# Kernel optimization log

Hardware: AMD Instinct MI355X
Metric: run time of the kernel (lower is better)

## Reference

```python
import jax, jax.numpy as jnp
import numpy as np

B, T, E, H, HD, FF = 2, 2048, 1024, 16, 64, 4096
LN_EPS = 1e-5


def _ln(x, g, b):
    mu = jnp.mean(x, axis=-1, keepdims=True)
    var = jnp.var(x, axis=-1, keepdims=True)
    return (x - mu) * jax.lax.rsqrt(var + LN_EPS) * g + b


def setup_inputs() -> dict:
    key = jax.random.key(0)
    ks = jax.random.split(key, 8)
    s = 0.02
    return {
        "x": jax.random.normal(ks[0], (B, T, E), jnp.float32),
        "Wq": jax.random.normal(ks[1], (H, E, HD), jnp.float32) * s,
        "Wk": jax.random.normal(ks[2], (H, E, HD), jnp.float32) * s,
        "Wv": jax.random.normal(ks[3], (H, E, HD), jnp.float32) * s,
        "Wproj": jax.random.normal(ks[4], (E, E), jnp.float32) * s,
        "bproj": jnp.zeros((E,), jnp.float32),
        "W1": jax.random.normal(ks[5], (E, FF), jnp.float32) * s,
        "b1": jnp.zeros((FF,), jnp.float32),
        "W2": jax.random.normal(ks[6], (FF, E), jnp.float32) * s,
        "b2": jnp.zeros((E,), jnp.float32),
        "g1": jnp.ones((E,), jnp.float32),
        "be1": jnp.zeros((E,), jnp.float32),
        "g2": jnp.ones((E,), jnp.float32),
        "be2": jnp.zeros((E,), jnp.float32),
    }


def reference(x, Wq, Wk, Wv, Wproj, bproj, W1, b1, W2, b2, g1, be1, g2, be2):
    # --- pre-LN multi-head causal self-attention (dropout = eval/identity) ---
    h = _ln(x, g1, be1)  # [B,T,E]
    q = jnp.einsum('btd,hde->bhte', h, Wq)  # [B,H,T,HD]
    k = jnp.einsum('btd,hde->bhte', h, Wk)
    v = jnp.einsum('btd,hde->bhte', h, Wv)
    # NOTE: original code scales by C**-0.5 where C = embedding_dim (not head_size)
    scale = E ** (-0.5)
    wei = jnp.einsum('bhqe,bhke->bhqk', q, k) * scale  # [B,H,T,T]
    causal = jnp.tril(jnp.ones((T, T), dtype=bool))
    wei = jnp.where(causal, wei, -jnp.inf)
    attn = jax.nn.softmax(wei, axis=-1)
    o = jnp.einsum('bhqk,bhke->bhqe', attn, v)  # [B,H,T,HD]
    o = o.transpose(0, 2, 1, 3).reshape(B, T, E)  # concat heads
    o = o @ Wproj + bproj
    x = x + o
    # --- ReLU FFN ---
    h2 = _ln(x, g2, be2)
    f = jax.nn.relu(h2 @ W1 + b1) @ W2 + b2
    return x + f
```

## Files before the change

kernel.cpp:

```cpp
#include <hip/hip_runtime.h>
#include <hip/hip_bf16.h>
#include <stdint.h>

#define T_SEQ 2048
#define E_DIM 1024
#define H_NUM 16
#define HD_DIM 64
#define FF_DIM 4096
#define B_NUM 2
#define N_TOK (B_NUM * T_SEQ)

typedef unsigned short ushort_t;
typedef __bf16 bf16x8 __attribute__((ext_vector_type(8)));
typedef float f32x4 __attribute__((ext_vector_type(4)));

__device__ __forceinline__ float bf2f(ushort_t u) {
    return __uint_as_float(((unsigned)u) << 16);
}
__device__ __forceinline__ ushort_t f2bf(float f) {
    unsigned u = __float_as_uint(f);
    u += 0x7fffu + ((u >> 16) & 1u);
    return (ushort_t)(u >> 16);
}
__device__ __forceinline__ float bflo(unsigned u) { return __uint_as_float(u << 16); }
__device__ __forceinline__ float bfhi(unsigned u) { return __uint_as_float(u & 0xffff0000u); }

__device__ __forceinline__ void async_copy16(const ushort_t* g, ushort_t* l) {
    __builtin_amdgcn_global_load_lds(
        (__attribute__((address_space(1))) uint32_t*)(ushort_t*)g,
        (__attribute__((address_space(3))) uint32_t*)l, 16, 0, 0);
}

__global__ __launch_bounds__(256) void ln_kernel(const float* __restrict__ x,
                                                 const float* __restrict__ g,
                                                 const float* __restrict__ be,
                                                 ushort_t* __restrict__ out) {
    __shared__ float red[8];
    const int row = blockIdx.x, tid = threadIdx.x;
    const float* xr = x + (size_t)row * E_DIM;
    float4 v = ((const float4*)xr)[tid];
    float s = v.x + v.y + v.z + v.w;
    float sq = v.x * v.x + v.y * v.y + v.z * v.z + v.w * v.w;
    for (int off = 32; off; off >>= 1) {
        s += __shfl_xor(s, off);
        sq += __shfl_xor(sq, off);
    }
    const int wid = tid >> 6, lane = tid & 63;
    if (lane == 0) { red[wid] = s; red[4 + wid] = sq; }
    __syncthreads();
    s = red[0] + red[1] + red[2] + red[3];
    sq = red[4] + red[5] + red[6] + red[7];
    const float mean = s * (1.0f / E_DIM);
    const float var = sq * (1.0f / E_DIM) - mean * mean;
    const float rstd = rsqrtf(var + 1e-5f);
    float4 gv = ((const float4*)g)[tid];
    float4 bv = ((const float4*)be)[tid];
    unsigned o0 = f2bf((v.x - mean) * rstd * gv.x + bv.x);
    unsigned o1 = f2bf((v.y - mean) * rstd * gv.y + bv.y);
    unsigned o2 = f2bf((v.z - mean) * rstd * gv.z + bv.z);
    unsigned o3 = f2bf((v.w - mean) * rstd * gv.w + bv.w);
    uint2 w;
    w.x = o0 | (o1 << 16);
    w.y = o2 | (o3 << 16);
    ((uint2*)(out + (size_t)row * E_DIM))[tid] = w;
}

__global__ __launch_bounds__(256) void reduce_ln_kernel(const ushort_t* __restrict__ p0,
                                                        const ushort_t* __restrict__ p1,
                                                        const float* __restrict__ x,
                                                        const float* __restrict__ bias,
                                                        const float* __restrict__ g,
                                                        const float* __restrict__ be,
                                                        float* __restrict__ x1,
                                                        ushort_t* __restrict__ h2) {
    __shared__ float red[8];
    const int row = blockIdx.x, tid = threadIdx.x;
    uint2 u0 = ((const uint2*)(p0 + (size_t)row * E_DIM))[tid];
    uint2 u1 = ((const uint2*)(p1 + (size_t)row * E_DIM))[tid];
    float4 xv = ((const float4*)(x + (size_t)row * E_DIM))[tid];
    float4 bv = ((const float4*)bias)[tid];
    float4 v;
    v.x = xv.x + bv.x + bflo(u0.x) + bflo(u1.x);
    v.y = xv.y + bv.y + bfhi(u0.x) + bfhi(u1.x);
    v.z = xv.z + bv.z + bflo(u0.y) + bflo(u1.y);
    v.w = xv.w + bv.w + bfhi(u0.y) + bfhi(u1.y);
    ((float4*)(x1 + (size_t)row * E_DIM))[tid] = v;
    float s = v.x + v.y + v.z + v.w;
    float sq = v.x * v.x + v.y * v.y + v.z * v.z + v.w * v.w;
    for (int off = 32; off; off >>= 1) {
        s += __shfl_xor(s, off);
        sq += __shfl_xor(sq, off);
    }
    const int wid = tid >> 6, lane = tid & 63;
    if (lane == 0) { red[wid] = s; red[4 + wid] = sq; }
    __syncthreads();
    s = red[0] + red[1] + red[2] + red[3];
    sq = red[4] + red[5] + red[6] + red[7];
    const float mean = s * (1.0f / E_DIM);
    const float var = sq * (1.0f / E_DIM) - mean * mean;
    const float rstd = rsqrtf(var + 1e-5f);
    float4 gv = ((const float4*)g)[tid];
    float4 ev = ((const float4*)be)[tid];
    unsigned o0 = f2bf((v.x - mean) * rstd * gv.x + ev.x);
    unsigned o1 = f2bf((v.y - mean) * rstd * gv.y + ev.y);
    unsigned o2 = f2bf((v.z - mean) * rstd * gv.z + ev.z);
    unsigned o3 = f2bf((v.w - mean) * rstd * gv.w + ev.w);
    uint2 w;
    w.x = o0 | (o1 << 16);
    w.y = o2 | (o3 << 16);
    ((uint2*)(h2 + (size_t)row * E_DIM))[tid] = w;
}

__global__ __launch_bounds__(256) void reduce_out_kernel(const ushort_t* __restrict__ p0,
                                                         const ushort_t* __restrict__ p1,
                                                         const float* __restrict__ x1,
                                                         const float* __restrict__ bias,
                                                         float* __restrict__ out) {
    const int row = blockIdx.x, tid = threadIdx.x;
    uint2 u0 = ((const uint2*)(p0 + (size_t)row * E_DIM))[tid];
    uint2 u1 = ((const uint2*)(p1 + (size_t)row * E_DIM))[tid];
    float4 xv = ((const float4*)(x1 + (size_t)row * E_DIM))[tid];
    float4 bv = ((const float4*)bias)[tid];
    float4 v;
    v.x = xv.x + bv.x + bflo(u0.x) + bflo(u1.x);
    v.y = xv.y + bv.y + bfhi(u0.x) + bfhi(u1.x);
    v.z = xv.z + bv.z + bflo(u0.y) + bflo(u1.y);
    v.w = xv.w + bv.w + bfhi(u0.y) + bfhi(u1.y);
    ((float4*)(out + (size_t)row * E_DIM))[tid] = v;
}

__global__ __launch_bounds__(256) void transpose_kernel(const float* __restrict__ in,
                                                        ushort_t* __restrict__ out,
                                                        int R, int C) {
    __shared__ ushort_t tile[32][33];
    const int c0 = blockIdx.x * 32, r0 = blockIdx.y * 32;
    const int tx = threadIdx.x, ty = threadIdx.y;
#pragma unroll
    for (int i = 0; i < 32; i += 8) tile[ty + i][tx] = f2bf(in[(size_t)(r0 + ty + i) * C + (c0 + tx)]);
    __syncthreads();
#pragma unroll
    for (int i = 0; i < 32; i += 8) out[(size_t)(c0 + ty + i) * R + (r0 + tx)] = tile[tx][ty + i];
}

__global__ __launch_bounds__(256) void transpose_qkv_kernel(const float* __restrict__ Wq,
                                                            const float* __restrict__ Wk,
                                                            const float* __restrict__ Wv,
                                                            ushort_t* __restrict__ outT) {
    __shared__ ushort_t tile[32][33];
    const int z = blockIdx.z, m = z >> 4, hh = z & 15;
    const float* in = ((m == 0) ? Wq : ((m == 1) ? Wk : Wv)) + (size_t)hh * E_DIM * HD_DIM;
    ushort_t* out = outT + (size_t)(m * E_DIM + hh * HD_DIM) * E_DIM;
    const int c0 = blockIdx.x * 32, r0 = blockIdx.y * 32;
    const int tx = threadIdx.x, ty = threadIdx.y;
#pragma unroll
    for (int i = 0; i < 32; i += 8) tile[ty + i][tx] = f2bf(in[(size_t)(r0 + ty + i) * HD_DIM + (c0 + tx)]);
    __syncthreads();
#pragma unroll
    for (int i = 0; i < 32; i += 8) out[(size_t)(c0 + ty + i) * E_DIM + (r0 + tx)] = tile[tx][ty + i];
}

template <int MODE, int BK>
__global__ __launch_bounds__(256) void gemm_bt(const ushort_t* __restrict__ A,
                                               const ushort_t* __restrict__ BT,
                                               const float* __restrict__ bias,
                                               const float* __restrict__ resid,
                                               void* __restrict__ C0,
                                               ushort_t* __restrict__ C1,
                                               ushort_t* __restrict__ C2,
                                               int M, int N, int K, int lda) {
    __shared__ __align__(16) ushort_t lds_a[2][128 * BK];
    __shared__ __align__(16) ushort_t lds_b[2][128 * BK];
    const int tid = threadIdx.x;
    const int id = blockIdx.y * gridDim.x + blockIdx.x;
    const int band = id & 7, within = id >> 3;
    const int rpb = gridDim.y >> 3;
    const int by = band * rpb + (within % rpb);
    const int bx = within / rpb;
    const int m0 = by * 128, n0 = bx * 128;
    const int koff = blockIdx.z * K;
    const int wave = tid >> 6, lane = tid & 63;
    const int wm = (wave >> 1) * 64, wn = (wave & 1) * 64;
    const int quad = lane >> 4, l16 = lane & 15;
    f32x4 acc[4][4] = {};

    const int nk = K / BK;
    auto stage = [&](int kt, int buf) {
        const int k0 = koff + kt * BK;
#pragma unroll
        for (int it = 0; it < BK / 16; ++it) {
            const int ci = it * 256 + tid;
            const int kk = ci >> 9;
            const int rem = ci & 511;
            const int r = rem >> 2, kc = rem & 3;
            const int gk = k0 + kk * 32 + kc * 8;
            async_copy16(A + (size_t)(m0 + r) * lda + gk, &lds_a[buf][ci * 8]);
            async_copy16(BT + (size_t)(n0 + r) * lda + gk, &lds_b[buf][ci * 8]);
        }
    };
    stage(0, 0);

#pragma unroll 1
    for (int kt = 0; kt < nk; ++kt) {
        __syncthreads();
        if (kt + 1 < nk) stage(kt + 1, (kt + 1) & 1);
        const ushort_t* la = lds_a[kt & 1];
        const ushort_t* lb = lds_b[kt & 1];
#pragma unroll
        for (int kk = 0; kk < BK / 32; ++kk) {
            const ushort_t* lak = la + kk * 4096;
            const ushort_t* lbk = lb + kk * 4096;
            bf16x8 af[4], bfr[4];
#pragma unroll
            for (int i = 0; i < 4; i++) af[i] = *(const bf16x8*)&lak[(wm + i * 16 + l16) * 32 + quad * 8];
#pragma unroll
            for (int i = 0; i < 4; i++) bfr[i] = *(const bf16x8*)&lbk[(wn + i * 16 + l16) * 32 + quad * 8];
#pragma unroll
            for (int im = 0; im < 4; im++)
#pragma unroll
                for (int in = 0; in < 4; in++)
                    acc[im][in] = __builtin_amdgcn_mfma_f32_16x16x32_bf16(af[im], bfr[in], acc[im][in], 0, 0, 0);
        }
    }

    ushort_t* pc = nullptr;
    if (MODE == 3) pc = (blockIdx.z == 0) ? (ushort_t*)C0 : C1;
#pragma unroll
    for (int im = 0; im < 4; im++) {
#pragma unroll
        for (int in = 0; in < 4; in++) {
            const int col = n0 + wn + in * 16 + l16;
            float bv = (MODE == 1 || MODE == 2) ? bias[col] : 0.0f;
#pragma unroll
            for (int r = 0; r < 4; r++) {
                const int row = m0 + wm + im * 16 + quad * 4 + r;
                float v = acc[im][in][r] + bv;
                if (MODE == 2) v = fmaxf(v, 0.0f);
                if (MODE == 1) v += resid[(size_t)row * N + col];
                if (MODE == 0) {
                    const int mat = col >> 10, c = col & 1023, hh = c >> 6, d = c & 63;
                    const int bb = row >> 11, tt = row & 2047;
                    const int bh = bb * H_NUM + hh;
                    size_t idx;
                    ushort_t* dst;
                    if (mat == 0) {
                        idx = ((((size_t)bh * 32 + (tt >> 6)) * 8 + (d >> 3)) * 64 + (tt & 63)) * 8 + (d & 7);
                        dst = (ushort_t*)C0;
                        v *= 0.0450842048f;
                    } else if (mat == 1) {
                        idx = ((((size_t)bh * 32 + (tt >> 6)) * 8 + (d >> 3)) * 64 + (tt & 63)) * 8 + (d & 7);
                        dst = C1;
                    } else {
                        idx = ((((size_t)bh * 32 + (tt >> 6)) * 8 + ((tt & 63) >> 3)) * 64 + d) * 8 + (tt & 7);
                        dst = C2;
                    }
                    dst[idx] = f2bf(v);
                } else if (MODE == 1) {
                    ((float*)C0)[(size_t)row * N + col] = v;
                } else if (MODE == 2) {
                    ((ushort_t*)C0)[(size_t)row * N + col] = f2bf(v);
                } else {
                    pc[(size_t)row * N + col] = f2bf(v);
                }
            }
        }
    }
    (void)M;
}

__global__ __launch_bounds__(256) void attn_flash(const ushort_t* __restrict__ qP,
                                                  const ushort_t* __restrict__ kP,
                                                  const ushort_t* __restrict__ vP,
                                                  ushort_t* __restrict__ o) {
    __shared__ __align__(16) ushort_t K_lds[2][4096];
    __shared__ __align__(16) ushort_t V_lds[2][4096];
    __shared__ __align__(16) ushort_t P_lds[4 * 16 * 72];
    const int h = blockIdx.x, p = blockIdx.y, b = blockIdx.z;
    const int bh = b * H_NUM + h;
    const int tid = threadIdx.x;
    const int wave = tid >> 6, lane = tid & 63;
    const int quad = lane >> 4, l16 = lane & 15;
    const int qrow0 = wave * 16;
    ushort_t* Pw = &P_lds[wave * 16 * 72];
    const ushort_t* kt_base = kP + (size_t)bh * 32 * 4096;
    const ushort_t* vt_base = vP + (size_t)bh * 32 * 4096;
    bf16x8 onesf;
#pragma unroll
    for (int j = 0; j < 8; ++j) onesf[j] = (__bf16)1.0f;

#pragma unroll 1
    for (int phase = 0; phase < 2; ++phase) {
        const int qt = (phase == 0) ? (31 - p) : p;
        const ushort_t* qbase = qP + ((size_t)bh * 32 + qt) * 4096;
        bf16x8 qf[2];
#pragma unroll
        for (int kk = 0; kk < 2; kk++)
            qf[kk] = *(const bf16x8*)&qbase[((kk * 4 + quad) * 64 + qrow0 + l16) * 8];
        f32x4 oacc[4] = {};
        f32x4 lacc = {};
        const int nkt = qt + 1;
        __syncthreads();
#pragma unroll
        for (int it = 0; it < 2; ++it) {
            const int ci = it * 256 + tid;
            async_copy16(kt_base + ci * 8, &K_lds[0][ci * 8]);
            async_copy16(vt_base + ci * 8, &V_lds[0][ci * 8]);
        }
#pragma unroll 1
        for (int kt = 0; kt < nkt; ++kt) {
            __syncthreads();
            if (kt + 1 < nkt) {
                const ushort_t* kn = kt_base + (size_t)(kt + 1) * 4096;
                const ushort_t* vn = vt_base + (size_t)(kt + 1) * 4096;
                ushort_t* kd = K_lds[(kt + 1) & 1];
                ushort_t* vd = V_lds[(kt + 1) & 1];
#pragma unroll
                for (int it = 0; it < 2; ++it) {
                    const int ci = it * 256 + tid;
                    async_copy16(kn + ci * 8, &kd[ci * 8]);
                    async_copy16(vn + ci * 8, &vd[ci * 8]);
                }
            }
            const ushort_t* Kb = K_lds[kt & 1];
            const ushort_t* Vb = V_lds[kt & 1];
            f32x4 sacc[4] = {};
#pragma unroll
            for (int kk = 0; kk < 2; kk++) {
                bf16x8 bfr[4];
#pragma unroll
                for (int in = 0; in < 4; in++)
                    bfr[in] = *(const bf16x8*)&Kb[(kk * 4 + quad) * 512 + (in * 16 + l16) * 8];
#pragma unroll
                for (int in = 0; in < 4; in++)
                    sacc[in] = __builtin_amdgcn_mfma_f32_16x16x32_bf16(qf[kk], bfr[in], sacc[in], 0, 0, 0);
            }
#pragma unroll
            for (int in = 0; in < 4; in++) {
                f32x4 sv = sacc[in];
                if (kt == qt) {
                    const int jc = in * 16 + l16;
#pragma unroll
                    for (int r = 0; r < 4; r++)
                        if (jc > qrow0 + quad * 4 + r) sv[r] = -3.0e38f;
                }
#pragma unroll
                for (int r = 0; r < 4; r++) {
                    const float e = exp2f(sv[r]);
                    Pw[(quad * 4 + r) * 72 + in * 16 + l16] =
                        (ushort_t)(__float_as_uint(e) >> 16);
                }
            }
#pragma unroll
            for (int kk = 0; kk < 2; kk++) {
                bf16x8 pf = *(const bf16x8*)&Pw[l16 * 72 + kk * 32 + quad * 8];
                lacc = __builtin_amdgcn_mfma_f32_16x16x32_bf16(pf, onesf, lacc, 0, 0, 0);
#pragma unroll
                for (int in = 0; in < 4; in++) {
                    bf16x8 vf = *(const bf16x8*)&Vb[(kk * 4 + quad) * 512 + (in * 16 + l16) * 8];
                    oacc[in] = __builtin_amdgcn_mfma_f32_16x16x32_bf16(pf, vf, oacc[in], 0, 0, 0);
                }
            }
        }
#pragma unroll
        for (int r = 0; r < 4; r++) {
            const float inv = 1.0f / lacc[r];
            const int trow = qt * 64 + qrow0 + quad * 4 + r;
#pragma unroll
            for (int in = 0; in < 4; in++) {
                o[(size_t)(b * T_SEQ + trow) * E_DIM + h * HD_DIM + in * 16 + l16] =
                    f2bf(oacc[in][r] * inv);
            }
        }
    }
}

extern "C" void kernel_launch(void* const* d_in, const int* in_sizes, int n_in,
                              void* d_out, int out_size, void* d_ws, size_t ws_size,
                              hipStream_t stream) {
    const float* x = (const float*)d_in[0];
    const float* Wq = (const float*)d_in[1];
    const float* Wk = (const float*)d_in[2];
    const float* Wv = (const float*)d_in[3];
    const float* Wproj = (const float*)d_in[4];
    const float* bproj = (const float*)d_in[5];
    const float* W1 = (const float*)d_in[6];
    const float* b1 = (const float*)d_in[7];
    const float* W2 = (const float*)d_in[8];
    const float* b2 = (const float*)d_in[9];
    const float* g1 = (const float*)d_in[10];
    const float* be1 = (const float*)d_in[11];
    const float* g2 = (const float*)d_in[12];
    const float* be2 = (const float*)d_in[13];

    char* ws = (char*)d_ws;
    const size_t MB = 1024 * 1024;
    ushort_t* W2T    = (ushort_t*)(ws + 0 * MB);
    float*    x1     = (float*)   (ws + 8 * MB);
    ushort_t* W1T    = (ushort_t*)(ws + 24 * MB);
    ushort_t* WprojT = (ushort_t*)(ws + 32 * MB);
    ushort_t* hln    = (ushort_t*)(ws + 34 * MB);
    ushort_t* ocat   = hln;
    ushort_t* WqkvT  = (ushort_t*)(ws + 42 * MB);
    ushort_t* qP     = (ushort_t*)(ws + 48 * MB);
    ushort_t* kP     = (ushort_t*)(ws + 56 * MB);
    ushort_t* vP     = (ushort_t*)(ws + 64 * MB);
    ushort_t* h2     = (ushort_t*)(ws + 72 * MB);
    ushort_t* f1     = (ushort_t*)(ws + 34 * MB);
    ushort_t* pp0    = (ushort_t*)(ws + 48 * MB);
    ushort_t* pp1    = (ushort_t*)(ws + 56 * MB);
    ushort_t* fp0    = (ushort_t*)(ws + 66 * MB);
    ushort_t* fp1    = (ushort_t*)(ws + 24 * MB);
    (void)ws_size; (void)in_sizes; (void)n_in; (void)out_size;

    const dim3 tb(32, 8, 1);
    transpose_qkv_kernel<<<dim3(2, 32, 48), tb, 0, stream>>>(Wq, Wk, Wv, WqkvT);
    transpose_kernel<<<dim3(32, 32, 1), tb, 0, stream>>>(Wproj, WprojT, E_DIM, E_DIM);
    transpose_kernel<<<dim3(128, 32, 1), tb, 0, stream>>>(W1, W1T, E_DIM, FF_DIM);
    transpose_kernel<<<dim3(32, 128, 1), tb, 0, stream>>>(W2, W2T, FF_DIM, E_DIM);

    ln_kernel<<<N_TOK, 256, 0, stream>>>(x, g1, be1, hln);
    gemm_bt<0, 32><<<dim3(24, 32), 256, 0, stream>>>(hln, WqkvT, nullptr, nullptr,
                                                     qP, kP, vP, N_TOK, 3 * E_DIM, E_DIM, E_DIM);
    attn_flash<<<dim3(16, 16, 2), 256, 0, stream>>>(qP, kP, vP, ocat);
    gemm_bt<3, 64><<<dim3(8, 32, 2), 256, 0, stream>>>(ocat, WprojT, nullptr, nullptr,
                                                       pp0, pp1, nullptr, N_TOK, E_DIM, 512, E_DIM);
    reduce_ln_kernel<<<N_TOK, 256, 0, stream>>>(pp0, pp1, x, bproj, g2, be2, x1, h2);
    gemm_bt<2, 64><<<dim3(32, 32), 256, 0, stream>>>(h2, W1T, b1, nullptr,
                                                     f1, nullptr, nullptr, N_TOK, FF_DIM, E_DIM, E_DIM);
    gemm_bt<3, 64><<<dim3(8, 32, 2), 256, 0, stream>>>(f1, W2T, nullptr, nullptr,
                                                       fp0, fp1, nullptr, N_TOK, E_DIM, 2048, FF_DIM);
    reduce_out_kernel<<<N_TOK, 256, 0, stream>>>(fp0, fp1, x1, b2, (float*)d_out);
}
```

Before: 336.7 us.

## Split attention KV tiles across wave pairs, loading K/V directly to registers

Reworks the flash-attention kernel so each wave handles 32 query rows and the two waves of a pair take alternate KV tiles, merging partial outputs and row sums through shared memory at the end. K and V are read straight from global memory into registers with a one-tile K prefetch, replacing the shared-memory double buffer and its per-tile barriers. MFMA sections are wrapped in s_setprio, and launch bounds request two blocks per CU. This aims to cut synchronisation and LDS traffic, and to double the MFMA work per K/V fragment loaded. The cost is higher register pressure and uncached per-wave global loads.

```diff
diff --git a/kernel.cpp b/kernel.cpp
--- a/kernel.cpp
+++ b/kernel.cpp
@@ -267,22 +267,22 @@
     (void)M;
 }
 
-__global__ __launch_bounds__(256) void attn_flash(const ushort_t* __restrict__ qP,
-                                                  const ushort_t* __restrict__ kP,
-                                                  const ushort_t* __restrict__ vP,
-                                                  ushort_t* __restrict__ o) {
-    __shared__ __align__(16) ushort_t K_lds[2][4096];
-    __shared__ __align__(16) ushort_t V_lds[2][4096];
-    __shared__ __align__(16) ushort_t P_lds[4 * 16 * 72];
+__global__ __launch_bounds__(256, 2) void attn_flash(const ushort_t* __restrict__ qP,
+                                                     const ushort_t* __restrict__ kP,
+                                                     const ushort_t* __restrict__ vP,
+                                                     ushort_t* __restrict__ o) {
+    __shared__ __align__(16) ushort_t P_lds[4][32 * 72];
+    __shared__ __align__(16) float Ored[2][32][68];
+    __shared__ float Lred[2][32];
     const int h = blockIdx.x, p = blockIdx.y, b = blockIdx.z;
     const int bh = b * H_NUM + h;
     const int tid = threadIdx.x;
     const int wave = tid >> 6, lane = tid & 63;
+    const int wr = wave >> 1, ws = wave & 1;
     const int quad = lane >> 4, l16 = lane & 15;
-    const int qrow0 = wave * 16;
-    ushort_t* Pw = &P_lds[wave * 16 * 72];
-    const ushort_t* kt_base = kP + (size_t)bh * 32 * 4096;
-    const ushort_t* vt_base = vP + (size_t)bh * 32 * 4096;
+    ushort_t* Pw = P_lds[wave];
+    const ushort_t* kbase = kP + (size_t)bh * 32 * 4096;
+    const ushort_t* vbase = vP + (size_t)bh * 32 * 4096;
     bf16x8 onesf;
 #pragma unroll
     for (int j = 0; j < 8; ++j) onesf[j] = (__bf16)1.0f;
@@ -290,85 +290,112 @@
 #pragma unroll 1
     for (int phase = 0; phase < 2; ++phase) {
         const int qt = (phase == 0) ? (31 - p) : p;
+        const int nkt = qt + 1;
         const ushort_t* qbase = qP + ((size_t)bh * 32 + qt) * 4096;
-        bf16x8 qf[2];
-#pragma unroll
-        for (int kk = 0; kk < 2; kk++)
-            qf[kk] = *(const bf16x8*)&qbase[((kk * 4 + quad) * 64 + qrow0 + l16) * 8];
-        f32x4 oacc[4] = {};
-        f32x4 lacc = {};
-        const int nkt = qt + 1;
+        bf16x8 qf[2][2];
+#pragma unroll
+        for (int rg = 0; rg < 2; ++rg)
+#pragma unroll
+            for (int kk = 0; kk < 2; ++kk)
+                qf[rg][kk] = *(const bf16x8*)&qbase[((kk * 4 + quad) * 64 + wr * 32 + rg * 16 + l16) * 8];
+        f32x4 oacc[2][4] = {};
+        f32x4 lacc[2] = {};
         __syncthreads();
-#pragma unroll
-        for (int it = 0; it < 2; ++it) {
-            const int ci = it * 256 + tid;
-            async_copy16(kt_base + ci * 8, &K_lds[0][ci * 8]);
-            async_copy16(vt_base + ci * 8, &V_lds[0][ci * 8]);
+        bf16x8 kf[8], vf[8];
+        {
+            const ushort_t* kb = kbase + (size_t)ws * 4096;
+#pragma unroll
+            for (int i = 0; i < 8; ++i)
+                kf[i] = *(const bf16x8*)&kb[(((i >> 2) * 4 + quad) * 64 + (i & 3) * 16 + l16) * 8];
         }
 #pragma unroll 1
-        for (int kt = 0; kt < nkt; ++kt) {
-            __syncthreads();
-            if (kt + 1 < nkt) {
-                const ushort_t* kn = kt_base + (size_t)(kt + 1) * 4096;
-                const ushort_t* vn = vt_base + (size_t)(kt + 1) * 4096;
-                ushort_t* kd = K_lds[(kt + 1) & 1];
-                ushort_t* vd = V_lds[(kt + 1) & 1];
-#pragma unroll
-                for (int it = 0; it < 2; ++it) {
-                    const int ci = it * 256 + tid;
-                    async_copy16(kn + ci * 8, &kd[ci * 8]);
-                    async_copy16(vn + ci * 8, &vd[ci * 8]);
+        for (int kt = ws; kt < nkt; kt += 2) {
+            f32x4 sacc[2][4] = {};
+            __builtin_amdgcn_s_setprio(1);
+#pragma unroll
+            for (int kk = 0; kk < 2; ++kk)
+#pragma unroll
+                for (int kg = 0; kg < 4; ++kg)
+#pragma unroll
+                    for (int rg = 0; rg < 2; ++rg)
+                        sacc[rg][kg] = __builtin_amdgcn_mfma_f32_16x16x32_bf16(
+                            qf[rg][kk], kf[kk * 4 + kg], sacc[rg][kg], 0, 0, 0);
+            __builtin_amdgcn_s_setprio(0);
+            {
+                const ushort_t* vb = vbase + (size_t)kt * 4096;
+#pragma unroll
+                for (int i = 0; i < 8; ++i)
+                    vf[i] = *(const bf16x8*)&vb[(((i >> 2) * 4 + quad) * 64 + (i & 3) * 16 + l16) * 8];
+            }
+            if (kt + 2 < nkt) {
+                const ushort_t* kb = kbase + (size_t)(kt + 2) * 4096;
+#pragma unroll
+                for (int i = 0; i < 8; ++i)
+                    kf[i] = *(const bf16x8*)&kb[(((i >> 2) * 4 + quad) * 64 + (i & 3) * 16 + l16) * 8];
+            }
+#pragma unroll
+            for (int rg = 0; rg < 2; ++rg)
+#pragma unroll
+                for (int kg = 0; kg < 4; ++kg) {
+                    f32x4 sv = sacc[rg][kg];
+                    if (kt == qt) {
+                        const int jc = kg * 16 + l16;
+#pragma unroll
+                        for (int r = 0; r < 4; ++r)
+                            if (jc > wr * 32 + rg * 16 + quad * 4 + r) sv[r] = -3.0e38f;
+                    }
+#pragma unroll
+                    for (int r = 0; r < 4; ++r) {
+                        const float e = exp2f(sv[r]);
+                        Pw[(rg * 16 + quad * 4 + r) * 72 + kg * 16 + l16] =
+                            (ushort_t)(__float_as_uint(e) >> 16);
+                    }
+                }
+            __builtin_amdgcn_s_setprio(1);
+#pragma unroll
+            for (int kk = 0; kk < 2; ++kk)
+#pragma unroll
+                for (int rg = 0; rg < 2; ++rg) {
+                    bf16x8 pf = *(const bf16x8*)&Pw[(rg * 16 + l16) * 72 + kk * 32 + quad * 8];
+                    lacc[rg] = __builtin_amdgcn_mfma_f32_16x16x32_bf16(pf, onesf, lacc[rg], 0, 0, 0);
+#pragma unroll
+                    for (int dg = 0; dg < 4; ++dg)
+                        oacc[rg][dg] = __builtin_amdgcn_mfma_f32_16x16x32_bf16(
+                            pf, vf[kk * 4 + dg], oacc[rg][dg], 0, 0, 0);
+                }
+            __builtin_amdgcn_s_setprio(0);
+        }
+        if (ws == 1) {
+#pragma unroll
+            for (int rg = 0; rg < 2; ++rg) {
+#pragma unroll
+                for (int dg = 0; dg < 4; ++dg)
+#pragma unroll
+                    for (int r = 0; r < 4; ++r)
+                        Ored[wr][rg * 16 + quad * 4 + r][dg * 16 + l16] = oacc[rg][dg][r];
+                if (l16 == 0) {
+#pragma unroll
+                    for (int r = 0; r < 4; ++r)
+                        Lred[wr][rg * 16 + quad * 4 + r] = lacc[rg][r];
                 }
             }
-            const ushort_t* Kb = K_lds[kt & 1];
-            const ushort_t* Vb = V_lds[kt & 1];
-            f32x4 sacc[4] = {};
-#pragma unroll
-            for (int kk = 0; kk < 2; kk++) {
-                bf16x8 bfr[4];
-#pragma unroll
-                for (int in = 0; in < 4; in++)
-                    bfr[in] = *(const bf16x8*)&Kb[(kk * 4 + quad) * 512 + (in * 16 + l16) * 8];
-#pragma unroll
-                for (int in = 0; in < 4; in++)
-                    sacc[in] = __builtin_amdgcn_mfma_f32_16x16x32_bf16(qf[kk], bfr[in], sacc[in], 0, 0, 0);
-            }
-#pragma unroll
-            for (int in = 0; in < 4; in++) {
-                f32x4 sv = sacc[in];
-                if (kt == qt) {
-                    const int jc = in * 16 + l16;
-#pragma unroll
-                    for (int r = 0; r < 4; r++)
-                        if (jc > qrow0 + quad * 4 + r) sv[r] = -3.0e38f;
+        }
+        __syncthreads();
+        if (ws == 0) {
+#pragma unroll
+            for (int rg = 0; rg < 2; ++rg)
+#pragma unroll
+                for (int r = 0; r < 4; ++r) {
+                    const int rr = rg * 16 + quad * 4 + r;
+                    const float inv = 1.0f / (lacc[rg][r] + Lred[wr][rr]);
+                    const int trow = qt * 64 + wr * 32 + rr;
+#pragma unroll
+                    for (int dg = 0; dg < 4; ++dg) {
+                        const float v = oacc[rg][dg][r] + Ored[wr][rr][dg * 16 + l16];
+                        o[(size_t)(b * T_SEQ + trow) * E_DIM + h * HD_DIM + dg * 16 + l16] =
+                            f2bf(v * inv);
+                    }
                 }
-#pragma unroll
-                for (int r = 0; r < 4; r++) {
-                    const float e = exp2f(sv[r]);
-                    Pw[(quad * 4 + r) * 72 + in * 16 + l16] =
-                        (ushort_t)(__float_as_uint(e) >> 16);
-                }
-            }
-#pragma unroll
-            for (int kk = 0; kk < 2; kk++) {
-                bf16x8 pf = *(const bf16x8*)&Pw[l16 * 72 + kk * 32 + quad * 8];
-                lacc = __builtin_amdgcn_mfma_f32_16x16x32_bf16(pf, onesf, lacc, 0, 0, 0);
-#pragma unroll
-                for (int in = 0; in < 4; in++) {
-                    bf16x8 vf = *(const bf16x8*)&Vb[(kk * 4 + quad) * 512 + (in * 16 + l16) * 8];
-                    oacc[in] = __builtin_amdgcn_mfma_f32_16x16x32_bf16(pf, vf, oacc[in], 0, 0, 0);
-                }
-            }
-        }
-#pragma unroll
-        for (int r = 0; r < 4; r++) {
-            const float inv = 1.0f / lacc[r];
-            const int trow = qt * 64 + qrow0 + quad * 4 + r;
-#pragma unroll
-            for (int in = 0; in < 4; in++) {
-                o[(size_t)(b * T_SEQ + trow) * E_DIM + h * HD_DIM + in * 16 + l16] =
-                    f2bf(oacc[in][r] * inv);
-            }
         }
     }
 }
```

Result: faster. 325.4 us (-3.3%).
